# Kernel tuning notes

Hardware: AMD Instinct MI355X
Metric: run time of the kernel (lower is better)

Reference implementation:

```python
import jax, jax.numpy as jnp
import numpy as np

B, N, E = 2, 2048, 1024
H = 16
D = E // H  # head dim = 64


def setup_inputs() -> dict:
    key = jax.random.key(0)
    ks = jax.random.split(key, 11)
    s = 1.0 / np.sqrt(E)
    return {
        "q": jax.random.normal(ks[0], (B, N, E), jnp.float32),
        "k": jax.random.normal(ks[1], (B, N, E), jnp.float32),
        "v": jax.random.normal(ks[2], (B, N, E), jnp.float32),
        "Wq": jax.random.normal(ks[3], (E, E), jnp.float32) * s,
        "bq": jnp.zeros((E,), jnp.float32),
        "Wk": jax.random.normal(ks[4], (E, E), jnp.float32) * s,
        "bk": jnp.zeros((E,), jnp.float32),
        "Wv": jax.random.normal(ks[5], (E, E), jnp.float32) * s,
        "bv": jnp.zeros((E,), jnp.float32),
        "Wo": jax.random.normal(ks[6], (E, E), jnp.float32) * s,
        "bo": jnp.zeros((E,), jnp.float32),
    }


def reference(q, k, v, Wq, bq, Wk, bk, Wv, bv, Wo, bo):
    # projections (torch Linear: x @ W^T + b)
    qp = q @ Wq.T + bq  # [B,N,E]
    kp = k @ Wk.T + bk
    vp = v @ Wv.T + bv
    # separate heads -> [B,H,N,D]
    qh = qp.reshape(B, N, H, D).transpose(0, 2, 1, 3)
    kh = kp.reshape(B, N, H, D).transpose(0, 2, 1, 3)
    vh = vp.reshape(B, N, H, D).transpose(0, 2, 1, 3)
    # scaled dot-product attention, full score matrix like the original
    scale = 1.0 / jnp.sqrt(jnp.asarray(D, qh.dtype))
    attn = jnp.einsum('bhqd,bhkd->bhqk', qh, kh) * scale
    attn = jax.nn.softmax(attn, axis=-1)
    out = jnp.einsum('bhqk,bhkd->bhqd', attn, vh)  # [B,H,N,D]
    # recombine heads
    out = out.transpose(0, 2, 1, 3).reshape(B, N, E)
    return out @ Wo.T + bo
```

## Files before the change

### kernel.cpp

```cpp
#include <hip/hip_runtime.h>

typedef _Float16 f16;
typedef __attribute__((ext_vector_type(2))) _Float16 f16x2;
typedef __attribute__((ext_vector_type(4))) _Float16 f16x4;
typedef __attribute__((ext_vector_type(8))) _Float16 f16x8;
typedef __attribute__((ext_vector_type(4))) float    f32x4;
typedef __attribute__((ext_vector_type(16))) float   f32x16;
typedef __attribute__((ext_vector_type(4))) unsigned u32x4;

static constexpr int B_ = 2, N_ = 2048, E_ = 1024, H_ = 16, D_ = 64;

#define MFMA16(a, b, c) __builtin_amdgcn_mfma_f32_16x16x32_f16(a, b, c, 0, 0, 0)
#define MFMA32(a, b, c) __builtin_amdgcn_mfma_f32_32x32x16_f16(a, b, c, 0, 0, 0)

#define QSCALE 0.18033688011112042f

__global__ __launch_bounds__(256) void castw_kernel(
    const float* __restrict__ Wq, const float* __restrict__ Wk,
    const float* __restrict__ Wv, const float* __restrict__ Wo,
    f16* __restrict__ dst)
{
    const int i = (blockIdx.x * 256 + threadIdx.x) * 4;
    const int which = i >> 20;
    const float* s = (which == 0) ? Wq : (which == 1) ? Wk : (which == 2) ? Wv : Wo;
    const int j = i & (E_ * E_ - 1);
    const f32x4 f = *(const f32x4*)&s[j];
    f16x4 o;
    o[0] = (f16)f[0]; o[1] = (f16)f[1]; o[2] = (f16)f[2]; o[3] = (f16)f[3];
    *(f16x4*)&dst[i] = o;
}

__global__ __launch_bounds__(256) void proj_gemm(
    const float* __restrict__ q, const float* __restrict__ k, const float* __restrict__ v,
    const f16* __restrict__ Wb,
    const float* __restrict__ bq, const float* __restrict__ bk, const float* __restrict__ bv,
    f16* __restrict__ qh, f16* __restrict__ kh, f16* __restrict__ vt)
{
    const int bid  = blockIdx.x;
    const int lin  = (bid & 7) * 96 + (bid >> 3);
    const int z    = lin >> 8;
    const int rem  = lin & 255;
    const int m0   = (rem >> 3) * 128;
    const int n0   = (rem & 7) * 128;

    const float* A    = (z == 0) ? q  : (z == 1) ? k  : v;
    const f16*   W    = Wb + (size_t)z * E_ * E_;
    const float* bias = (z == 0) ? bq : (z == 1) ? bk : bv;

    __shared__ f16 As[128][40];
    __shared__ f16 Bs[128][40];

    const int tid  = threadIdx.x;
    const int lane = tid & 63, w = tid >> 6;
    const int lr = lane & 15, lg = lane >> 4;
    const int wm = (w >> 1) * 64, wn = (w & 1) * 64;

    const int srow = tid >> 1;
    const int skh  = (tid & 1) * 16;

    f32x4 acc[4][4];
#pragma unroll
    for (int i = 0; i < 4; i++)
#pragma unroll
        for (int j = 0; j < 4; j++) acc[i][j] = (f32x4){0.f, 0.f, 0.f, 0.f};

    for (int k0 = 0; k0 < E_; k0 += 32) {
        __syncthreads();
        {
            const float* src = &A[(size_t)(m0 + srow) * E_ + k0 + skh];
            const f32x4 f0 = *(const f32x4*)(src + 0);
            const f32x4 f1 = *(const f32x4*)(src + 4);
            const f32x4 f2 = *(const f32x4*)(src + 8);
            const f32x4 f3 = *(const f32x4*)(src + 12);
            f16x8 b0, b1;
#pragma unroll
            for (int t = 0; t < 4; t++) { b0[t] = (f16)f0[t]; b0[4 + t] = (f16)f1[t]; }
#pragma unroll
            for (int t = 0; t < 4; t++) { b1[t] = (f16)f2[t]; b1[4 + t] = (f16)f3[t]; }
            *(f16x8*)&As[srow][skh]     = b0;
            *(f16x8*)&As[srow][skh + 8] = b1;
        }
        {
            const f16* src = &W[(size_t)(n0 + srow) * E_ + k0 + skh];
            *(f16x8*)&Bs[srow][skh]     = *(const f16x8*)(src);
            *(f16x8*)&Bs[srow][skh + 8] = *(const f16x8*)(src + 8);
        }
        __syncthreads();

        f16x8 af[4], bfr[4];
#pragma unroll
        for (int ms = 0; ms < 4; ms++) af[ms]  = *(const f16x8*)&As[wm + ms * 16 + lr][lg * 8];
#pragma unroll
        for (int ns = 0; ns < 4; ns++) bfr[ns] = *(const f16x8*)&Bs[wn + ns * 16 + lr][lg * 8];
#pragma unroll
        for (int ms = 0; ms < 4; ms++)
#pragma unroll
            for (int ns = 0; ns < 4; ns++)
                acc[ms][ns] = MFMA16(af[ms], bfr[ns], acc[ms][ns]);
    }

    const float oscale = (z == 0) ? QSCALE : 1.0f;
#pragma unroll
    for (int ms = 0; ms < 4; ms++) {
        const int mbase = m0 + wm + ms * 16 + lg * 4;
#pragma unroll
        for (int ns = 0; ns < 4; ns++) {
            const int n  = n0 + wn + ns * 16 + lr;
            const float bn = bias[n];
            const int hh = n >> 6, dd = n & 63;
#pragma unroll
            for (int r = 0; r < 4; r++) {
                const float val = (acc[ms][ns][r] + bn) * oscale;
                const int mm = mbase + r;
                const int bb = mm >> 11;
                const int nn = mm & (N_ - 1);
                if (z == 2) {
                    vt[((size_t)(bb * H_ + hh) * D_ + dd) * N_ + nn] = (f16)val;
                } else {
                    f16* dst = (z == 0) ? qh : kh;
                    dst[((size_t)(bb * H_ + hh) * N_ + nn) * D_ + dd] = (f16)val;
                }
            }
        }
    }
}

__global__ __launch_bounds__(256) void attn_kernel(
    const f16* __restrict__ qh, const f16* __restrict__ kh,
    const f16* __restrict__ vt, f16* __restrict__ ao)
{
    const int bid = blockIdx.x;
    const int swz = (bid & 7) * 64 + (bid >> 3);
    const int qt = swz & 15;
    const int bh = swz >> 4;

    const int tid = threadIdx.x;
    const int w = tid >> 6, lane = tid & 63;
    const int l31 = lane & 31;
    const bool hi = (lane >> 5) != 0;
    const int hib = hi ? 1 : 0;

    const f16* qp = qh + (size_t)bh * N_ * D_;
    const f16* kp = kh + (size_t)bh * N_ * D_;
    const f16* vp = vt + (size_t)bh * D_ * N_;

    const int qrow = qt * 128 + w * 32 + l31;

    f16x8 qf[4];
#pragma unroll
    for (int ks = 0; ks < 4; ks++)
        qf[ks] = *(const f16x8*)&qp[(size_t)qrow * D_ + ks * 16 + hib * 8];

    __shared__ f16 Ks[2][64][64];
    __shared__ f16 Vs[2][64][64];

    const int srow = tid >> 3;
    const int sch  = tid & 7;
    const int ssl  = (sch ^ (srow & 7)) * 8;

    const f16* kg0 = kp + (size_t)srow * D_ + sch * 8;
    const f16* kg1 = kg0 + (size_t)32 * D_;
    const f16* vg0 = vp + (size_t)srow * N_ + sch * 8;
    const f16* vg1 = vg0 + (size_t)32 * N_;

    f32x16 oT0 = {0.f,0.f,0.f,0.f,0.f,0.f,0.f,0.f,0.f,0.f,0.f,0.f,0.f,0.f,0.f,0.f};
    f32x16 oT1 = oT0;
    float mrun = -3.0e38f, lrun = 0.f;

    f16x8 kr0 = *(const f16x8*)(kg0);
    f16x8 kr1 = *(const f16x8*)(kg1);
    f16x8 vr0 = *(const f16x8*)(vg0);
    f16x8 vr1 = *(const f16x8*)(vg1);

    constexpr int NT = N_ / 64;
    int cur = 0;

    for (int t = 0; t < NT; ++t) {
        *(f16x8*)&Ks[cur][srow     ][ssl] = kr0;
        *(f16x8*)&Ks[cur][srow + 32][ssl] = kr1;
        *(f16x8*)&Vs[cur][srow     ][ssl] = vr0;
        *(f16x8*)&Vs[cur][srow + 32][ssl] = vr1;
        if (t + 1 < NT) {
            kr0 = *(const f16x8*)(kg0 + (size_t)(t + 1) * 64 * D_);
            kr1 = *(const f16x8*)(kg1 + (size_t)(t + 1) * 64 * D_);
            vr0 = *(const f16x8*)(vg0 + (t + 1) * 64);
            vr1 = *(const f16x8*)(vg1 + (t + 1) * 64);
        }
        __syncthreads();

        f32x16 sA = {0.f,0.f,0.f,0.f,0.f,0.f,0.f,0.f,0.f,0.f,0.f,0.f,0.f,0.f,0.f,0.f};
        f32x16 sB = sA;
        __builtin_amdgcn_s_setprio(1);
#pragma unroll
        for (int ks = 0; ks < 4; ks++) {
            const int c = (ks * 2 + hib) ^ (l31 & 7);
            const f16x8 kfA = *(const f16x8*)&Ks[cur][l31     ][c * 8];
            const f16x8 kfB = *(const f16x8*)&Ks[cur][l31 + 32][c * 8];
            sA = MFMA32(kfA, qf[ks], sA);
            sB = MFMA32(kfB, qf[ks], sB);
        }
        __builtin_amdgcn_s_setprio(0);

        float tt[16];
#pragma unroll
        for (int r = 0; r < 16; r++) tt[r] = fmaxf(sA[r], sB[r]);
#pragma unroll
        for (int d = 8; d >= 1; d >>= 1)
#pragma unroll
            for (int r = 0; r < d; r++) tt[r] = fmaxf(tt[r], tt[r + d]);
        float pmax = fmaxf(tt[0], __shfl_xor(tt[0], 32));

        if (!__all(pmax - mrun <= 8.0f)) {
            const float mnew = fmaxf(mrun, pmax);
            const float alpha = __builtin_amdgcn_exp2f(mrun - mnew);
            mrun = mnew;
            lrun *= alpha;
#pragma unroll
            for (int r = 0; r < 16; r++) { oT0[r] *= alpha; oT1[r] *= alpha; }
        }

        float p0 = 0.f, p1 = 0.f, p2 = 0.f, p3 = 0.f;
#pragma unroll
        for (int r = 0; r < 16; r += 4) {
            sA[r]   = __builtin_amdgcn_exp2f(sA[r]   - mrun); p0 += sA[r];
            sA[r+1] = __builtin_amdgcn_exp2f(sA[r+1] - mrun); p1 += sA[r+1];
            sA[r+2] = __builtin_amdgcn_exp2f(sA[r+2] - mrun); p2 += sA[r+2];
            sA[r+3] = __builtin_amdgcn_exp2f(sA[r+3] - mrun); p3 += sA[r+3];
        }
#pragma unroll
        for (int r = 0; r < 16; r += 4) {
            sB[r]   = __builtin_amdgcn_exp2f(sB[r]   - mrun); p0 += sB[r];
            sB[r+1] = __builtin_amdgcn_exp2f(sB[r+1] - mrun); p1 += sB[r+1];
            sB[r+2] = __builtin_amdgcn_exp2f(sB[r+2] - mrun); p2 += sB[r+2];
            sB[r+3] = __builtin_amdgcn_exp2f(sB[r+3] - mrun); p3 += sB[r+3];
        }
        float lsum = (p0 + p1) + (p2 + p3);
        lsum += __shfl_xor(lsum, 32);
        lrun += lsum;

        __builtin_amdgcn_s_setprio(1);
#define PVSTEP(PP0,PP1,PP2,PP3,PP4,PP5,PP6,PP7, KSI)                                   \
        {                                                                              \
            const unsigned w0 = __builtin_bit_cast(unsigned, __builtin_amdgcn_cvt_pkrtz(PP0, PP1)); \
            const unsigned w1 = __builtin_bit_cast(unsigned, __builtin_amdgcn_cvt_pkrtz(PP2, PP3)); \
            const unsigned w2 = __builtin_bit_cast(unsigned, __builtin_amdgcn_cvt_pkrtz(PP4, PP5)); \
            const unsigned w3 = __builtin_bit_cast(unsigned, __builtin_amdgcn_cvt_pkrtz(PP6, PP7)); \
            const unsigned x0 = (unsigned)__shfl_xor((int)w0, 32);                     \
            const unsigned x1 = (unsigned)__shfl_xor((int)w1, 32);                     \
            const unsigned x2 = (unsigned)__shfl_xor((int)w2, 32);                     \
            const unsigned x3 = (unsigned)__shfl_xor((int)w3, 32);                     \
            u32x4 pw;                                                                  \
            pw[0] = hi ? x2 : w0;                                                      \
            pw[1] = hi ? x3 : w1;                                                      \
            pw[2] = hi ? w2 : x0;                                                      \
            pw[3] = hi ? w3 : x1;                                                      \
            const f16x8 pa = __builtin_bit_cast(f16x8, pw);                            \
            const int c = ((KSI) * 2 + hib) ^ (l31 & 7);                               \
            const f16x8 vf0 = *(const f16x8*)&Vs[cur][l31     ][c * 8];                \
            const f16x8 vf1 = *(const f16x8*)&Vs[cur][l31 + 32][c * 8];                \
            oT0 = MFMA32(vf0, pa, oT0);                                                \
            oT1 = MFMA32(vf1, pa, oT1);                                                \
        }
        PVSTEP(sA[0],sA[1],sA[2],sA[3],sA[4],sA[5],sA[6],sA[7], 0)
        PVSTEP(sA[8],sA[9],sA[10],sA[11],sA[12],sA[13],sA[14],sA[15], 1)
        PVSTEP(sB[0],sB[1],sB[2],sB[3],sB[4],sB[5],sB[6],sB[7], 2)
        PVSTEP(sB[8],sB[9],sB[10],sB[11],sB[12],sB[13],sB[14],sB[15], 3)
#undef PVSTEP
        __builtin_amdgcn_s_setprio(0);

        cur ^= 1;
    }

    const float inv = 1.0f / lrun;
    const int b = bh >> 4, h = bh & 15;
    f16* dst = ao + (size_t)(b * N_ + qrow) * E_ + h * 64 + hib * 4;
#pragma unroll
    for (int g = 0; g < 4; g++) {
        f16x4 o0, o1;
#pragma unroll
        for (int j = 0; j < 4; j++) {
            o0[j] = (f16)(oT0[g * 4 + j] * inv);
            o1[j] = (f16)(oT1[g * 4 + j] * inv);
        }
        *(f16x4*)&dst[8 * g]      = o0;
        *(f16x4*)&dst[8 * g + 32] = o1;
    }
}

__global__ __launch_bounds__(256) void out_gemm(
    const f16* __restrict__ ao, const f16* __restrict__ Wo,
    const float* __restrict__ bo, float* __restrict__ out)
{
    __shared__ f16 As[128][40];
    __shared__ f16 Bs[128][40];

    const int bid = blockIdx.x;
    const int lin = (bid & 7) * 32 + (bid >> 3);
    const int m0  = (lin >> 3) * 128;
    const int n0  = (lin & 7) * 128;

    const int tid  = threadIdx.x;
    const int lane = tid & 63, w = tid >> 6;
    const int lr = lane & 15, lg = lane >> 4;
    const int wm = (w >> 1) * 64, wn = (w & 1) * 64;

    const int srow = tid >> 1;
    const int skh  = (tid & 1) * 16;

    f32x4 acc[4][4];
#pragma unroll
    for (int i = 0; i < 4; i++)
#pragma unroll
        for (int j = 0; j < 4; j++) acc[i][j] = (f32x4){0.f, 0.f, 0.f, 0.f};

    for (int k0 = 0; k0 < E_; k0 += 32) {
        __syncthreads();
        {
            const f16* src = &ao[(size_t)(m0 + srow) * E_ + k0 + skh];
            *(f16x8*)&As[srow][skh]     = *(const f16x8*)(src);
            *(f16x8*)&As[srow][skh + 8] = *(const f16x8*)(src + 8);
        }
        {
            const f16* src = &Wo[(size_t)(n0 + srow) * E_ + k0 + skh];
            *(f16x8*)&Bs[srow][skh]     = *(const f16x8*)(src);
            *(f16x8*)&Bs[srow][skh + 8] = *(const f16x8*)(src + 8);
        }
        __syncthreads();

        f16x8 af[4], bfr[4];
#pragma unroll
        for (int ms = 0; ms < 4; ms++) af[ms]  = *(const f16x8*)&As[wm + ms * 16 + lr][lg * 8];
#pragma unroll
        for (int ns = 0; ns < 4; ns++) bfr[ns] = *(const f16x8*)&Bs[wn + ns * 16 + lr][lg * 8];
#pragma unroll
        for (int ms = 0; ms < 4; ms++)
#pragma unroll
            for (int ns = 0; ns < 4; ns++)
                acc[ms][ns] = MFMA16(af[ms], bfr[ns], acc[ms][ns]);
    }

#pragma unroll
    for (int ms = 0; ms < 4; ms++) {
        const int mbase = m0 + wm + ms * 16 + lg * 4;
#pragma unroll
        for (int ns = 0; ns < 4; ns++) {
            const int n = n0 + wn + ns * 16 + lr;
            const float bn = bo[n];
#pragma unroll
            for (int r = 0; r < 4; r++) {
                out[(size_t)(mbase + r) * E_ + n] = acc[ms][ns][r] + bn;
            }
        }
    }
}

extern "C" void kernel_launch(void* const* d_in, const int* in_sizes, int n_in,
                              void* d_out, int out_size, void* d_ws, size_t ws_size,
                              hipStream_t stream) {
    const float* q  = (const float*)d_in[0];
    const float* k  = (const float*)d_in[1];
    const float* v  = (const float*)d_in[2];
    const float* Wq = (const float*)d_in[3];
    const float* bq = (const float*)d_in[4];
    const float* Wk = (const float*)d_in[5];
    const float* bk = (const float*)d_in[6];
    const float* Wv = (const float*)d_in[7];
    const float* bv = (const float*)d_in[8];
    const float* Wo = (const float*)d_in[9];
    const float* bo = (const float*)d_in[10];
    float* out = (float*)d_out;

    char* ws = (char*)d_ws;
    f16* Wb = (f16*)ws;
    f16* qh = (f16*)(ws + (size_t) 8 * 1024 * 1024);
    f16* kh = (f16*)(ws + (size_t)16 * 1024 * 1024);
    f16* vt = (f16*)(ws + (size_t)24 * 1024 * 1024);
    f16* ao = (f16*)(ws + (size_t)32 * 1024 * 1024);

    castw_kernel<<<4096, 256, 0, stream>>>(Wq, Wk, Wv, Wo, Wb);
    proj_gemm<<<768, 256, 0, stream>>>(q, k, v, Wb, bq, bk, bv, qh, kh, vt);
    attn_kernel<<<512, 256, 0, stream>>>(qh, kh, vt, ao);
    out_gemm<<<256, 256, 0, stream>>>(ao, Wb + (size_t)3 * E_ * E_, bo, out);
}
```

Measured before the change: 155.0 us.

## Pre-cast activations to fp16 and load GEMM tiles via direct global-to-LDS with XOR swizzle

The q/k/v activations are now cast to fp16 in the same pre-pass that casts the weights, so the projection GEMM reads fp16 instead of converting fp32 in its inner loop. Both GEMMs now fill shared memory with global_load_lds 16-byte direct transfers into unpadded tiles, using an XOR swizzle on the column chunk to avoid bank conflicts. The MFMA block is wrapped in s_setprio raises. The cost is an extra full read and write of the activations to workspace, which adds traffic that has to be paid back by a cheaper GEMM inner loop.

Measured after the change: 149.7 us. 3.4% less time.

```diff
diff --git a/kernel.cpp b/kernel.cpp
--- a/kernel.cpp
+++ b/kernel.cpp
@@ -9,21 +9,38 @@
 typedef __attribute__((ext_vector_type(4))) unsigned u32x4;
 
 static constexpr int B_ = 2, N_ = 2048, E_ = 1024, H_ = 16, D_ = 64;
+static constexpr int M_ = B_ * N_;
 
 #define MFMA16(a, b, c) __builtin_amdgcn_mfma_f32_16x16x32_f16(a, b, c, 0, 0, 0)
 #define MFMA32(a, b, c) __builtin_amdgcn_mfma_f32_32x32x16_f16(a, b, c, 0, 0, 0)
 
 #define QSCALE 0.18033688011112042f
 
-__global__ __launch_bounds__(256) void castw_kernel(
+__device__ __forceinline__ void gload_lds16(const f16* g, f16* l) {
+    typedef __attribute__((address_space(1))) const unsigned gu32;
+    typedef __attribute__((address_space(3))) unsigned       lu32;
+    __builtin_amdgcn_global_load_lds((gu32*)g, (lu32*)l, 16, 0, 0);
+}
+
+__global__ __launch_bounds__(256) void cast_all(
     const float* __restrict__ Wq, const float* __restrict__ Wk,
     const float* __restrict__ Wv, const float* __restrict__ Wo,
-    f16* __restrict__ dst)
+    const float* __restrict__ q, const float* __restrict__ k,
+    const float* __restrict__ v, f16* __restrict__ dst)
 {
     const int i = (blockIdx.x * 256 + threadIdx.x) * 4;
-    const int which = i >> 20;
-    const float* s = (which == 0) ? Wq : (which == 1) ? Wk : (which == 2) ? Wv : Wo;
-    const int j = i & (E_ * E_ - 1);
+    const float* s;
+    int j;
+    if (i < 4 * E_ * E_) {
+        const int which = i >> 20;
+        s = (which == 0) ? Wq : (which == 1) ? Wk : (which == 2) ? Wv : Wo;
+        j = i & (E_ * E_ - 1);
+    } else {
+        const int t = i - 4 * E_ * E_;
+        const int which = t >> 22;
+        s = (which == 0) ? q : (which == 1) ? k : v;
+        j = t & (M_ * E_ - 1);
+    }
     const f32x4 f = *(const f32x4*)&s[j];
     f16x4 o;
     o[0] = (f16)f[0]; o[1] = (f16)f[1]; o[2] = (f16)f[2]; o[3] = (f16)f[3];
@@ -31,8 +48,7 @@
 }
 
 __global__ __launch_bounds__(256) void proj_gemm(
-    const float* __restrict__ q, const float* __restrict__ k, const float* __restrict__ v,
-    const f16* __restrict__ Wb,
+    const f16* __restrict__ Aall, const f16* __restrict__ Wb,
     const float* __restrict__ bq, const float* __restrict__ bk, const float* __restrict__ bv,
     f16* __restrict__ qh, f16* __restrict__ kh, f16* __restrict__ vt)
 {
@@ -43,20 +59,27 @@
     const int m0   = (rem >> 3) * 128;
     const int n0   = (rem & 7) * 128;
 
-    const float* A    = (z == 0) ? q  : (z == 1) ? k  : v;
-    const f16*   W    = Wb + (size_t)z * E_ * E_;
+    const f16* A    = Aall + (size_t)z * M_ * E_;
+    const f16* W    = Wb + (size_t)z * E_ * E_;
     const float* bias = (z == 0) ? bq : (z == 1) ? bk : bv;
 
-    __shared__ f16 As[128][40];
-    __shared__ f16 Bs[128][40];
+    __shared__ f16 As[128][32];
+    __shared__ f16 Bs[128][32];
 
     const int tid  = threadIdx.x;
     const int lane = tid & 63, w = tid >> 6;
     const int lr = lane & 15, lg = lane >> 4;
     const int wm = (w >> 1) * 64, wn = (w & 1) * 64;
 
-    const int srow = tid >> 1;
-    const int skh  = (tid & 1) * 16;
+    const int gch = ((lane & 3) ^ ((lane >> 3) & 3)) * 8;
+    const f16* ag = A + (size_t)(m0 + w * 32 + (lane >> 2)) * E_ + gch;
+    const f16* bg = W + (size_t)(n0 + w * 32 + (lane >> 2)) * E_ + gch;
+    f16* al0 = &As[w * 32][0];
+    f16* al1 = &As[w * 32 + 16][0];
+    f16* bl0 = &Bs[w * 32][0];
+    f16* bl1 = &Bs[w * 32 + 16][0];
+
+    const int ca = (lg ^ ((lr >> 1) & 3)) * 8;
 
     f32x4 acc[4][4];
 #pragma unroll
@@ -64,39 +87,27 @@
 #pragma unroll
         for (int j = 0; j < 4; j++) acc[i][j] = (f32x4){0.f, 0.f, 0.f, 0.f};
 
-    for (int k0 = 0; k0 < E_; k0 += 32) {
+    for (int t = 0; t < E_ / 32; ++t) {
         __syncthreads();
-        {
-            const float* src = &A[(size_t)(m0 + srow) * E_ + k0 + skh];
-            const f32x4 f0 = *(const f32x4*)(src + 0);
-            const f32x4 f1 = *(const f32x4*)(src + 4);
-            const f32x4 f2 = *(const f32x4*)(src + 8);
-            const f32x4 f3 = *(const f32x4*)(src + 12);
-            f16x8 b0, b1;
-#pragma unroll
-            for (int t = 0; t < 4; t++) { b0[t] = (f16)f0[t]; b0[4 + t] = (f16)f1[t]; }
-#pragma unroll
-            for (int t = 0; t < 4; t++) { b1[t] = (f16)f2[t]; b1[4 + t] = (f16)f3[t]; }
-            *(f16x8*)&As[srow][skh]     = b0;
-            *(f16x8*)&As[srow][skh + 8] = b1;
-        }
-        {
-            const f16* src = &W[(size_t)(n0 + srow) * E_ + k0 + skh];
-            *(f16x8*)&Bs[srow][skh]     = *(const f16x8*)(src);
-            *(f16x8*)&Bs[srow][skh + 8] = *(const f16x8*)(src + 8);
-        }
+        gload_lds16(ag,                 al0);
+        gload_lds16(ag + 16 * E_,       al1);
+        gload_lds16(bg,                 bl0);
+        gload_lds16(bg + 16 * E_,       bl1);
+        ag += 32; bg += 32;
         __syncthreads();
 
         f16x8 af[4], bfr[4];
 #pragma unroll
-        for (int ms = 0; ms < 4; ms++) af[ms]  = *(const f16x8*)&As[wm + ms * 16 + lr][lg * 8];
-#pragma unroll
-        for (int ns = 0; ns < 4; ns++) bfr[ns] = *(const f16x8*)&Bs[wn + ns * 16 + lr][lg * 8];
+        for (int ms = 0; ms < 4; ms++) af[ms]  = *(const f16x8*)&As[wm + ms * 16 + lr][ca];
+#pragma unroll
+        for (int ns = 0; ns < 4; ns++) bfr[ns] = *(const f16x8*)&Bs[wn + ns * 16 + lr][ca];
+        __builtin_amdgcn_s_setprio(1);
 #pragma unroll
         for (int ms = 0; ms < 4; ms++)
 #pragma unroll
             for (int ns = 0; ns < 4; ns++)
                 acc[ms][ns] = MFMA16(af[ms], bfr[ns], acc[ms][ns]);
+        __builtin_amdgcn_s_setprio(0);
     }
 
     const float oscale = (z == 0) ? QSCALE : 1.0f;
@@ -291,8 +302,8 @@
     const f16* __restrict__ ao, const f16* __restrict__ Wo,
     const float* __restrict__ bo, float* __restrict__ out)
 {
-    __shared__ f16 As[128][40];
-    __shared__ f16 Bs[128][40];
+    __shared__ f16 As[128][32];
+    __shared__ f16 Bs[128][32];
 
     const int bid = blockIdx.x;
     const int lin = (bid & 7) * 32 + (bid >> 3);
@@ -304,8 +315,15 @@
     const int lr = lane & 15, lg = lane >> 4;
     const int wm = (w >> 1) * 64, wn = (w & 1) * 64;
 
-    const int srow = tid >> 1;
-    const int skh  = (tid & 1) * 16;
+    const int gch = ((lane & 3) ^ ((lane >> 3) & 3)) * 8;
+    const f16* ag = ao + (size_t)(m0 + w * 32 + (lane >> 2)) * E_ + gch;
+    const f16* bg = Wo + (size_t)(n0 + w * 32 + (lane >> 2)) * E_ + gch;
+    f16* al0 = &As[w * 32][0];
+    f16* al1 = &As[w * 32 + 16][0];
+    f16* bl0 = &Bs[w * 32][0];
+    f16* bl1 = &Bs[w * 32 + 16][0];
+
+    const int ca = (lg ^ ((lr >> 1) & 3)) * 8;
 
     f32x4 acc[4][4];
 #pragma unroll
@@ -313,30 +331,27 @@
 #pragma unroll
         for (int j = 0; j < 4; j++) acc[i][j] = (f32x4){0.f, 0.f, 0.f, 0.f};
 
-    for (int k0 = 0; k0 < E_; k0 += 32) {
+    for (int t = 0; t < E_ / 32; ++t) {
         __syncthreads();
-        {
-            const f16* src = &ao[(size_t)(m0 + srow) * E_ + k0 + skh];
-            *(f16x8*)&As[srow][skh]     = *(const f16x8*)(src);
-            *(f16x8*)&As[srow][skh + 8] = *(const f16x8*)(src + 8);
-        }
-        {
-            const f16* src = &Wo[(size_t)(n0 + srow) * E_ + k0 + skh];
-            *(f16x8*)&Bs[srow][skh]     = *(const f16x8*)(src);
-            *(f16x8*)&Bs[srow][skh + 8] = *(const f16x8*)(src + 8);
-        }
+        gload_lds16(ag,            al0);
+        gload_lds16(ag + 16 * E_,  al1);
+        gload_lds16(bg,            bl0);
+        gload_lds16(bg + 16 * E_,  bl1);
+        ag += 32; bg += 32;
         __syncthreads();
 
         f16x8 af[4], bfr[4];
 #pragma unroll
-        for (int ms = 0; ms < 4; ms++) af[ms]  = *(const f16x8*)&As[wm + ms * 16 + lr][lg * 8];
-#pragma unroll
-        for (int ns = 0; ns < 4; ns++) bfr[ns] = *(const f16x8*)&Bs[wn + ns * 16 + lr][lg * 8];
+        for (int ms = 0; ms < 4; ms++) af[ms]  = *(const f16x8*)&As[wm + ms * 16 + lr][ca];
+#pragma unroll
+        for (int ns = 0; ns < 4; ns++) bfr[ns] = *(const f16x8*)&Bs[wn + ns * 16 + lr][ca];
+        __builtin_amdgcn_s_setprio(1);
 #pragma unroll
         for (int ms = 0; ms < 4; ms++)
 #pragma unroll
             for (int ns = 0; ns < 4; ns++)
                 acc[ms][ns] = MFMA16(af[ms], bfr[ns], acc[ms][ns]);
+        __builtin_amdgcn_s_setprio(0);
     }
 
 #pragma unroll
@@ -371,14 +386,16 @@
     float* out = (float*)d_out;
 
     char* ws = (char*)d_ws;
-    f16* Wb = (f16*)ws;
-    f16* qh = (f16*)(ws + (size_t) 8 * 1024 * 1024);
-    f16* kh = (f16*)(ws + (size_t)16 * 1024 * 1024);
-    f16* vt = (f16*)(ws + (size_t)24 * 1024 * 1024);
-    f16* ao = (f16*)(ws + (size_t)32 * 1024 * 1024);
-
-    castw_kernel<<<4096, 256, 0, stream>>>(Wq, Wk, Wv, Wo, Wb);
-    proj_gemm<<<768, 256, 0, stream>>>(q, k, v, Wb, bq, bk, bv, qh, kh, vt);
+    f16* cast = (f16*)ws;
+    f16* Wb   = cast;
+    f16* Aall = cast + (size_t)4 * E_ * E_;
+    f16* qh = (f16*)(ws + (size_t)32 * 1024 * 1024);
+    f16* kh = (f16*)(ws + (size_t)40 * 1024 * 1024);
+    f16* vt = (f16*)(ws + (size_t)48 * 1024 * 1024);
+    f16* ao = (f16*)(ws + (size_t)56 * 1024 * 1024);
+
+    cast_all<<<16384, 256, 0, stream>>>(Wq, Wk, Wv, Wo, q, k, v, cast);
+    proj_gemm<<<768, 256, 0, stream>>>(Aall, Wb, bq, bk, bv, qh, kh, vt);
     attn_kernel<<<512, 256, 0, stream>>>(qh, kh, vt, ao);
     out_gemm<<<256, 256, 0, stream>>>(ao, Wb + (size_t)3 * E_ * E_, bo, out);
 }
```
